# Performance work log

Hardware: AMD Instinct MI355X
Metric: run time of the kernel (lower is better)

Reference implementation:

```python
import jax, jax.numpy as jnp
import numpy as np


def setup_inputs() -> dict:
    key = jax.random.key(0)
    k1, k2 = jax.random.split(key)
    B, Tq, Tk, D = 16, 1024, 1024, 1024
    decoder_hidden = jax.random.normal(k1, (B, Tq, D), dtype=jnp.float32)
    encoder_outputs = jax.random.normal(k2, (B, Tk, D), dtype=jnp.float32)
    return {"decoder_hidden": decoder_hidden, "encoder_outputs": encoder_outputs}


def reference(decoder_hidden, encoder_outputs):
    # Unscaled Luong dot-product attention: bmm -> softmax -> bmm
    # scores: [B, Tq, Tk]
    scores = jnp.einsum("bqd,bkd->bqk", decoder_hidden, encoder_outputs)
    weights = jax.nn.softmax(scores, axis=-1)
    # context: [B, Tq, D]
    return jnp.einsum("bqk,bkd->bqd", weights, encoder_outputs)
```

## Files before the change

### kernel.cpp

```cpp
#include <hip/hip_runtime.h>
#include <hip/hip_fp16.h>
#include <stdint.h>


typedef _Float16 half_t;
typedef __attribute__((ext_vector_type(8))) _Float16 f16x8;
typedef __attribute__((ext_vector_type(4))) float f32x4;

__global__ __launch_bounds__(256) void cvt_kernel(
    const float* __restrict__ enc,
    half_t* __restrict__ encsw, half_t* __restrict__ encTsw) {
    __shared__ half_t lt[64 * 65];
    const int b = blockIdx.z;
    const int rt = blockIdx.x, ct = blockIdx.y;
    const int t = threadIdx.x;
    const int r = t >> 2;
    const int c0 = (t & 3) << 4;
    const size_t bofs = (size_t)b << 20;

    const float* src = enc + bofs + (size_t)(rt * 64 + r) * 1024 + ct * 64 + c0;
    const float4* s4 = (const float4*)src;
    const float4 f0 = s4[0];
    const float4 f1 = s4[1];
    const float4 f2 = s4[2];
    const float4 f3 = s4[3];

    union { half_t h[16]; uint4 q[2]; } v;
    v.h[0]  = (half_t)f0.x; v.h[1]  = (half_t)f0.y;
    v.h[2]  = (half_t)f0.z; v.h[3]  = (half_t)f0.w;
    v.h[4]  = (half_t)f1.x; v.h[5]  = (half_t)f1.y;
    v.h[6]  = (half_t)f1.z; v.h[7]  = (half_t)f1.w;
    v.h[8]  = (half_t)f2.x; v.h[9]  = (half_t)f2.y;
    v.h[10] = (half_t)f2.z; v.h[11] = (half_t)f2.w;
    v.h[12] = (half_t)f3.x; v.h[13] = (half_t)f3.y;
    v.h[14] = (half_t)f3.z; v.h[15] = (half_t)f3.w;

    {
        const int gr = rt * 64 + r, gc = ct * 64 + c0;
        half_t* dst = encsw + bofs
                      + (size_t)(gc >> 5) * 32768 + gr * 32 + (gc & 31);
        ((uint4*)dst)[0] = v.q[0];
        ((uint4*)dst)[1] = v.q[1];
    }

#pragma unroll
    for (int i = 0; i < 16; ++i) lt[r * 65 + c0 + i] = v.h[i];
    __syncthreads();
    union { half_t h[16]; uint4 q[2]; } w;
#pragma unroll
    for (int i = 0; i < 16; ++i) w.h[i] = lt[(c0 + i) * 65 + r];
    const int gk = rt * 64 + c0, gd = ct * 64 + r;
    half_t* dstT = encTsw + bofs
                   + (size_t)(gk >> 5) * 32768 + gd * 32 + (gk & 31);
    ((uint4*)dstT)[0] = w.q[0];
    ((uint4*)dstT)[1] = w.q[1];
}

__global__ __launch_bounds__(512, 2) void scores_kernel(
    const float* __restrict__ dec, const half_t* __restrict__ encsw,
    half_t* __restrict__ p16) {
    __shared__ __align__(16) unsigned char smem[65536];
    half_t* qlds = (half_t*)smem;
    float* red = (float*)smem;
    float* redg = (float*)(smem + 2048);

    const int l = blockIdx.x;
    const int xcd = l & 7, idx = l >> 3;
    const int b = xcd + ((idx >> 4) << 3);
    const int qbase = (idx & 15) * 64;

    const int tid = threadIdx.x;
    const int w = tid >> 6, lane = tid & 63, quad = lane >> 4, n16 = lane & 15;
    const int laneoff = n16 * 32 + quad * 8;
    const size_t bofs = (size_t)b << 20;

    const int sr = tid >> 3;
    const int sp = tid & 7;
    const int sg = (sr >> 1) & 3;
    const float* srcrow = dec + bofs + (size_t)(qbase + sr) * 1024;

    int aoff[4];
#pragma unroll
    for (int rb = 0; rb < 4; ++rb) {
        const int lr = rb * 16 + n16;
        aoff[rb] = lr * 32 + ((quad ^ ((lr >> 1) & 3)) << 3);
    }

    f32x4 acc[4][8];
#pragma unroll
    for (int rb = 0; rb < 4; ++rb)
#pragma unroll
        for (int cf = 0; cf < 8; ++cf) acc[rb][cf] = (f32x4){0.f, 0.f, 0.f, 0.f};

#pragma unroll
    for (int ph = 0; ph < 2; ++ph) {
        if (ph) __syncthreads();
#pragma unroll
        for (int k = 0; k < 4; ++k) {
            const int c0 = sp * 16 + k * 128;
            const float4* spv = (const float4*)(srcrow + ph * 512 + c0);
            const float4 a0 = spv[0], a1 = spv[1], a2 = spv[2], a3 = spv[3];
            union { half_t h[16]; uint4 q[2]; } u;
            u.h[0]  = (half_t)a0.x; u.h[1]  = (half_t)a0.y;
            u.h[2]  = (half_t)a0.z; u.h[3]  = (half_t)a0.w;
            u.h[4]  = (half_t)a1.x; u.h[5]  = (half_t)a1.y;
            u.h[6]  = (half_t)a1.z; u.h[7]  = (half_t)a1.w;
            u.h[8]  = (half_t)a2.x; u.h[9]  = (half_t)a2.y;
            u.h[10] = (half_t)a2.z; u.h[11] = (half_t)a2.w;
            u.h[12] = (half_t)a3.x; u.h[13] = (half_t)a3.y;
            u.h[14] = (half_t)a3.z; u.h[15] = (half_t)a3.w;
            const int chunk = c0 >> 5;
            const int s0 = (c0 & 31) >> 3;
            half_t* base = qlds + chunk * 2048 + sr * 32;
            ((uint4*)(base + ((s0 ^ sg) << 3)))[0] = u.q[0];
            ((uint4*)(base + (((s0 + 1) ^ sg) << 3)))[0] = u.q[1];
        }
        __syncthreads();

        for (int dcl = 0; dcl < 16; ++dcl) {
            const int dc = ph * 16 + dcl;
            const half_t* ec = encsw + bofs + (size_t)dc * 32768;
            f16x8 bf[8];
#pragma unroll
            for (int h = 0; h < 2; ++h)
#pragma unroll
                for (int cb = 0; cb < 4; ++cb)
                    bf[h * 4 + cb] = *(const f16x8*)(
                        ec + (h * 512 + w * 64 + cb * 16) * 32 + laneoff);
            f16x8 af[4];
#pragma unroll
            for (int rb = 0; rb < 4; ++rb)
                af[rb] = *(const f16x8*)(qlds + dcl * 2048 + aoff[rb]);
#pragma unroll
            for (int rb = 0; rb < 4; ++rb)
#pragma unroll
                for (int cf = 0; cf < 8; ++cf)
                    acc[rb][cf] = __builtin_amdgcn_mfma_f32_16x16x32_f16(
                        af[rb], bf[cf], acc[rb][cf], 0, 0, 0);
        }
    }
    __syncthreads();

    float mrow[4][4], srow[4][4];
#pragma unroll
    for (int rb = 0; rb < 4; ++rb)
#pragma unroll
        for (int r = 0; r < 4; ++r) {
            float m = -1e30f;
#pragma unroll
            for (int cf = 0; cf < 8; ++cf) m = fmaxf(m, acc[rb][cf][r]);
#pragma unroll
            for (int off = 1; off < 16; off <<= 1)
                m = fmaxf(m, __shfl_xor(m, off, 64));
            mrow[rb][r] = m;
        }
    if (n16 == 0) {
#pragma unroll
        for (int rb = 0; rb < 4; ++rb)
#pragma unroll
            for (int r = 0; r < 4; ++r)
                red[w * 64 + rb * 16 + quad * 4 + r] = mrow[rb][r];
    }
    __syncthreads();
    if (tid < 64) {
        float g = red[tid];
#pragma unroll
        for (int ww = 1; ww < 8; ++ww) g = fmaxf(g, red[ww * 64 + tid]);
        redg[tid] = g;
    }
    __syncthreads();
#pragma unroll
    for (int rb = 0; rb < 4; ++rb)
#pragma unroll
        for (int r = 0; r < 4; ++r) mrow[rb][r] = redg[rb * 16 + quad * 4 + r];
    __syncthreads();

#pragma unroll
    for (int rb = 0; rb < 4; ++rb)
#pragma unroll
        for (int r = 0; r < 4; ++r) {
            float s = 0.f;
#pragma unroll
            for (int cf = 0; cf < 8; ++cf) {
                float p = __expf(acc[rb][cf][r] - mrow[rb][r]);
                acc[rb][cf][r] = p;
                s += p;
            }
#pragma unroll
            for (int off = 1; off < 16; off <<= 1) s += __shfl_xor(s, off, 64);
            srow[rb][r] = s;
        }
    if (n16 == 0) {
#pragma unroll
        for (int rb = 0; rb < 4; ++rb)
#pragma unroll
            for (int r = 0; r < 4; ++r)
                red[w * 64 + rb * 16 + quad * 4 + r] = srow[rb][r];
    }
    __syncthreads();
    if (tid < 64) {
        float g = 0.f;
#pragma unroll
        for (int ww = 0; ww < 8; ++ww) g += red[ww * 64 + tid];
        redg[tid] = g;
    }
    __syncthreads();
#pragma unroll
    for (int rb = 0; rb < 4; ++rb)
#pragma unroll
        for (int r = 0; r < 4; ++r)
            srow[rb][r] = 1.0f / redg[rb * 16 + quad * 4 + r];

#pragma unroll
    for (int rb = 0; rb < 4; ++rb)
#pragma unroll
        for (int cf = 0; cf < 8; ++cf) {
            const int colbase = ((cf >> 2) << 9) + w * 64 + ((cf & 3) << 4);
            half_t* pp = p16 + bofs + (size_t)(colbase >> 5) * 32768
                         + (colbase & 31) + n16;
#pragma unroll
            for (int r = 0; r < 4; ++r) {
                const int row = qbase + rb * 16 + quad * 4 + r;
                pp[row * 32] = (half_t)(acc[rb][cf][r] * srow[rb][r]);
            }
        }
}

__global__ __launch_bounds__(256, 2) void ctx_kernel(
    const half_t* __restrict__ p16, const half_t* __restrict__ encTsw,
    float* __restrict__ out) {
    const int l = blockIdx.x;
    const int xcd = l & 7, idx = l >> 3;
    const int b = xcd + ((idx >> 5) << 3);
    const int rem = idx & 31;
    const int qt = rem >> 2, dt = rem & 3;
    const int tid = threadIdx.x;
    const int w = tid >> 6, lane = tid & 63, quad = lane >> 4, n16 = lane & 15;
    const int wr = w >> 1, wc = w & 1;
    const int laneoff = n16 * 32 + quad * 8;
    const size_t bofs = (size_t)b << 20;

    const int arow0 = qt * 128 + wr * 64;
    const int brow0 = dt * 256 + wc * 128;

    f32x4 acc[4][8];
#pragma unroll
    for (int i = 0; i < 4; ++i)
#pragma unroll
        for (int j = 0; j < 8; ++j) acc[i][j] = (f32x4){0.f, 0.f, 0.f, 0.f};

    for (int kc = 0; kc < 32; ++kc) {
        const half_t* ac = p16 + bofs + (size_t)kc * 32768;
        const half_t* bc = encTsw + bofs + (size_t)kc * 32768;
        f16x8 af[4], bf[8];
#pragma unroll
        for (int rb = 0; rb < 4; ++rb)
            af[rb] = *(const f16x8*)(ac + (arow0 + rb * 16) * 32 + laneoff);
#pragma unroll
        for (int cb = 0; cb < 8; ++cb)
            bf[cb] = *(const f16x8*)(bc + (brow0 + cb * 16) * 32 + laneoff);
#pragma unroll
        for (int rb = 0; rb < 4; ++rb)
#pragma unroll
            for (int cb = 0; cb < 8; ++cb)
                acc[rb][cb] = __builtin_amdgcn_mfma_f32_16x16x32_f16(
                    af[rb], bf[cb], acc[rb][cb], 0, 0, 0);
    }

#pragma unroll
    for (int rb = 0; rb < 4; ++rb)
#pragma unroll
        for (int cb = 0; cb < 8; ++cb)
#pragma unroll
            for (int r = 0; r < 4; ++r) {
                const int row = arow0 + rb * 16 + quad * 4 + r;
                const int col = brow0 + cb * 16 + n16;
                out[bofs + (size_t)row * 1024 + col] = acc[rb][cb][r];
            }
}

extern "C" void kernel_launch(void* const* d_in, const int* in_sizes, int n_in,
                              void* d_out, int out_size, void* d_ws, size_t ws_size,
                              hipStream_t stream) {
    (void)in_sizes; (void)n_in; (void)out_size; (void)ws_size;
    const float* dec = (const float*)d_in[0];
    const float* enc = (const float*)d_in[1];
    float* out = (float*)d_out;

    half_t* p16    = (half_t*)d_ws;
    half_t* encsw  = p16 + ((size_t)16 << 20);
    half_t* encTsw = encsw + ((size_t)16 << 20);

    cvt_kernel<<<dim3(16, 16, 16), 256, 0, stream>>>(enc, encsw, encTsw);
    scores_kernel<<<dim3(256), 512, 0, stream>>>(dec, encsw, p16);
    ctx_kernel<<<dim3(512), 256, 0, stream>>>(p16, encTsw, out);
}
```

Measured before the change: 266.5 us.

## Fuse scores and context GEMMs into one kernel via LDS-staged probabilities

Merges the scores/softmax kernel and the context GEMM into a single kernel. Normalized fp16 probabilities are staged in LDS in two halves, so the global p16 round trip and one launch go away. The cost is a 256-block grid of 512 threads, where the old ctx kernel used 512 blocks, so parallelism drops. It also raises register pressure from holding the second half of the probabilities plus a new 4x8 accumulator array. Each block's second GEMM reads all of encTsw for its batch from global memory with no LDS sharing of B.

```diff
diff --git a/kernel.cpp b/kernel.cpp
--- a/kernel.cpp
+++ b/kernel.cpp
@@ -5,6 +5,7 @@
 
 typedef _Float16 half_t;
 typedef __attribute__((ext_vector_type(8))) _Float16 f16x8;
+typedef __attribute__((ext_vector_type(2))) _Float16 f16x2;
 typedef __attribute__((ext_vector_type(4))) float f32x4;
 
 __global__ __launch_bounds__(256) void cvt_kernel(
@@ -56,11 +57,12 @@
     ((uint4*)dstT)[1] = w.q[1];
 }
 
-__global__ __launch_bounds__(512, 2) void scores_kernel(
+__global__ __launch_bounds__(512, 2) void fused_kernel(
     const float* __restrict__ dec, const half_t* __restrict__ encsw,
-    half_t* __restrict__ p16) {
+    const half_t* __restrict__ encTsw, float* __restrict__ out) {
     __shared__ __align__(16) unsigned char smem[65536];
     half_t* qlds = (half_t*)smem;
+    half_t* plds = (half_t*)smem;
     float* red = (float*)smem;
     float* redg = (float*)(smem + 2048);
 
@@ -211,71 +213,108 @@
         for (int r = 0; r < 4; ++r)
             srow[rb][r] = 1.0f / redg[rb * 16 + quad * 4 + r];
 
-#pragma unroll
-    for (int rb = 0; rb < 4; ++rb)
-#pragma unroll
-        for (int cf = 0; cf < 8; ++cf) {
-            const int colbase = ((cf >> 2) << 9) + w * 64 + ((cf & 3) << 4);
-            half_t* pp = p16 + bofs + (size_t)(colbase >> 5) * 32768
-                         + (colbase & 31) + n16;
+    f16x2 hp[4][4][2];
+#pragma unroll
+    for (int rb = 0; rb < 4; ++rb)
+#pragma unroll
+        for (int cb = 0; cb < 4; ++cb)
+#pragma unroll
+            for (int pr = 0; pr < 2; ++pr) {
+                f16x2 t;
+                t[0] = (half_t)(acc[rb][4 + cb][2 * pr] * srow[rb][2 * pr]);
+                t[1] = (half_t)(acc[rb][4 + cb][2 * pr + 1] * srow[rb][2 * pr + 1]);
+                hp[rb][cb][pr] = t;
+            }
+    __syncthreads();
+
+#pragma unroll
+    for (int rb = 0; rb < 4; ++rb)
+#pragma unroll
+        for (int cb = 0; cb < 4; ++cb) {
+            const int cl = w * 64 + cb * 16 + n16;
+            const int chunk = cl >> 5;
+            const int l8 = (cl & 31) >> 3;
+            const int c7 = cl & 7;
+#pragma unroll
+            for (int r = 0; r < 4; ++r) {
+                const int lr = rb * 16 + quad * 4 + r;
+                const int g = (lr >> 1) & 3;
+                plds[chunk * 2048 + lr * 32 + (((l8 ^ g)) << 3) + c7] =
+                    (half_t)(acc[rb][cb][r] * srow[rb][r]);
+            }
+        }
+    __syncthreads();
+
+    f32x4 accv[4][8];
+#pragma unroll
+    for (int rb = 0; rb < 4; ++rb)
+#pragma unroll
+        for (int cb = 0; cb < 8; ++cb) accv[rb][cb] = (f32x4){0.f, 0.f, 0.f, 0.f};
+
+    for (int kcl = 0; kcl < 16; ++kcl) {
+        const half_t* tc = encTsw + bofs + (size_t)kcl * 32768;
+        f16x8 bf[8];
+#pragma unroll
+        for (int cb = 0; cb < 8; ++cb)
+            bf[cb] = *(const f16x8*)(tc + (w * 128 + cb * 16) * 32 + laneoff);
+        f16x8 af[4];
+#pragma unroll
+        for (int rb = 0; rb < 4; ++rb)
+            af[rb] = *(const f16x8*)(plds + kcl * 2048 + aoff[rb]);
+#pragma unroll
+        for (int rb = 0; rb < 4; ++rb)
+#pragma unroll
+            for (int cb = 0; cb < 8; ++cb)
+                accv[rb][cb] = __builtin_amdgcn_mfma_f32_16x16x32_f16(
+                    af[rb], bf[cb], accv[rb][cb], 0, 0, 0);
+    }
+    __syncthreads();
+
+#pragma unroll
+    for (int rb = 0; rb < 4; ++rb)
+#pragma unroll
+        for (int cb = 0; cb < 4; ++cb) {
+            const int cl = w * 64 + cb * 16 + n16;
+            const int chunk = cl >> 5;
+            const int l8 = (cl & 31) >> 3;
+            const int c7 = cl & 7;
+#pragma unroll
+            for (int r = 0; r < 4; ++r) {
+                const int lr = rb * 16 + quad * 4 + r;
+                const int g = (lr >> 1) & 3;
+                plds[chunk * 2048 + lr * 32 + (((l8 ^ g)) << 3) + c7] =
+                    hp[rb][cb][r >> 1][r & 1];
+            }
+        }
+    __syncthreads();
+
+    for (int kcl = 0; kcl < 16; ++kcl) {
+        const half_t* tc = encTsw + bofs + (size_t)(16 + kcl) * 32768;
+        f16x8 bf[8];
+#pragma unroll
+        for (int cb = 0; cb < 8; ++cb)
+            bf[cb] = *(const f16x8*)(tc + (w * 128 + cb * 16) * 32 + laneoff);
+        f16x8 af[4];
+#pragma unroll
+        for (int rb = 0; rb < 4; ++rb)
+            af[rb] = *(const f16x8*)(plds + kcl * 2048 + aoff[rb]);
+#pragma unroll
+        for (int rb = 0; rb < 4; ++rb)
+#pragma unroll
+            for (int cb = 0; cb < 8; ++cb)
+                accv[rb][cb] = __builtin_amdgcn_mfma_f32_16x16x32_f16(
+                    af[rb], bf[cb], accv[rb][cb], 0, 0, 0);
+    }
+
+#pragma unroll
+    for (int rb = 0; rb < 4; ++rb)
+#pragma unroll
+        for (int cb = 0; cb < 8; ++cb)
 #pragma unroll
             for (int r = 0; r < 4; ++r) {
                 const int row = qbase + rb * 16 + quad * 4 + r;
-                pp[row * 32] = (half_t)(acc[rb][cf][r] * srow[rb][r]);
-            }
-        }
-}
-
-__global__ __launch_bounds__(256, 2) void ctx_kernel(
-    const half_t* __restrict__ p16, const half_t* __restrict__ encTsw,
-    float* __restrict__ out) {
-    const int l = blockIdx.x;
-    const int xcd = l & 7, idx = l >> 3;
-    const int b = xcd + ((idx >> 5) << 3);
-    const int rem = idx & 31;
-    const int qt = rem >> 2, dt = rem & 3;
-    const int tid = threadIdx.x;
-    const int w = tid >> 6, lane = tid & 63, quad = lane >> 4, n16 = lane & 15;
-    const int wr = w >> 1, wc = w & 1;
-    const int laneoff = n16 * 32 + quad * 8;
-    const size_t bofs = (size_t)b << 20;
-
-    const int arow0 = qt * 128 + wr * 64;
-    const int brow0 = dt * 256 + wc * 128;
-
-    f32x4 acc[4][8];
-#pragma unroll
-    for (int i = 0; i < 4; ++i)
-#pragma unroll
-        for (int j = 0; j < 8; ++j) acc[i][j] = (f32x4){0.f, 0.f, 0.f, 0.f};
-
-    for (int kc = 0; kc < 32; ++kc) {
-        const half_t* ac = p16 + bofs + (size_t)kc * 32768;
-        const half_t* bc = encTsw + bofs + (size_t)kc * 32768;
-        f16x8 af[4], bf[8];
-#pragma unroll
-        for (int rb = 0; rb < 4; ++rb)
-            af[rb] = *(const f16x8*)(ac + (arow0 + rb * 16) * 32 + laneoff);
-#pragma unroll
-        for (int cb = 0; cb < 8; ++cb)
-            bf[cb] = *(const f16x8*)(bc + (brow0 + cb * 16) * 32 + laneoff);
-#pragma unroll
-        for (int rb = 0; rb < 4; ++rb)
-#pragma unroll
-            for (int cb = 0; cb < 8; ++cb)
-                acc[rb][cb] = __builtin_amdgcn_mfma_f32_16x16x32_f16(
-                    af[rb], bf[cb], acc[rb][cb], 0, 0, 0);
-    }
-
-#pragma unroll
-    for (int rb = 0; rb < 4; ++rb)
-#pragma unroll
-        for (int cb = 0; cb < 8; ++cb)
-#pragma unroll
-            for (int r = 0; r < 4; ++r) {
-                const int row = arow0 + rb * 16 + quad * 4 + r;
-                const int col = brow0 + cb * 16 + n16;
-                out[bofs + (size_t)row * 1024 + col] = acc[rb][cb][r];
+                const int col = w * 128 + cb * 16 + n16;
+                out[bofs + (size_t)row * 1024 + col] = accv[rb][cb][r];
             }
 }
 
@@ -287,11 +326,9 @@
     const float* enc = (const float*)d_in[1];
     float* out = (float*)d_out;
 
-    half_t* p16    = (half_t*)d_ws;
-    half_t* encsw  = p16 + ((size_t)16 << 20);
+    half_t* encsw  = (half_t*)d_ws;
     half_t* encTsw = encsw + ((size_t)16 << 20);
 
     cvt_kernel<<<dim3(16, 16, 16), 256, 0, stream>>>(enc, encsw, encTsw);
-    scores_kernel<<<dim3(256), 512, 0, stream>>>(dec, encsw, p16);
-    ctx_kernel<<<dim3(512), 256, 0, stream>>>(p16, encTsw, out);
+    fused_kernel<<<dim3(256), 512, 0, stream>>>(dec, encsw, encTsw, out);
 }
```

Result: slower. 278.9 us (+4.7%).
